# Kernel tuning notes

Measured on AMD Instinct MI355X. Metric: run time of the kernel, lower is better.

## Reference

```python
import jax, jax.numpy as jnp
import numpy as np

N, D, F, M, K = 4096, 1024, 4096, 2048, 307
EPS = 1e-5

def _ln(h, g, b):
    mu = jnp.mean(h, axis=-1, keepdims=True)
    var = jnp.mean(jnp.square(h - mu), axis=-1, keepdims=True)
    return (h - mu) * jax.lax.rsqrt(var + EPS) * g + b

def _attn(h, wq, wk, wv, mask):
    # wq/wk/wv stored as [D, D] so y = h @ w matches torch Linear(h) with W.T
    q = h @ wq
    k = h @ wk
    v = h @ wv
    s = (q @ k.T) * (1.0 / np.sqrt(D))  # [N, N]
    s = jnp.where(mask, -1e9, s)
    a = jax.nn.softmax(s, axis=-1)
    return a @ v, a

def _ffn(h, w1, b1, w2, b2):
    return jax.nn.gelu(h @ w1 + b1, approximate=False) @ w2 + b2

def setup_inputs() -> dict:
    ks = jax.random.split(jax.random.key(0), 32)
    s = 0.02
    p = lambda i, shape: (jax.random.normal(ks[i], shape, jnp.float32) * s)
    inp = {
        'x': jax.random.normal(ks[0], (N, D), jnp.float32),
        'real_edge_mask': jax.random.bernoulli(ks[1], 0.5, (N, N)),
        'fake_edge_mask': jax.random.bernoulli(ks[2], 0.5, (N, N)),
        'mask_nodes': jax.random.permutation(ks[3], N)[:M].astype(jnp.int32),
        'gene_idx': jnp.argsort(jax.random.uniform(ks[4], (M, D)), axis=-1)[:, :K].astype(jnp.int32),
        'wq1': p(5, (D, D)), 'wk1': p(6, (D, D)), 'wv1': p(7, (D, D)),
        'g1': jnp.ones((D,)), 'be1': jnp.zeros((D,)),
        'fw1': p(8, (D, F)), 'fb1': jnp.zeros((F,)),
        'fw2': p(9, (F, D)), 'fb2': jnp.zeros((D,)),
        'g2': jnp.ones((D,)), 'be2': jnp.zeros((D,)),
        'wq2': p(10, (D, D)), 'wk2': p(11, (D, D)), 'wv2': p(12, (D, D)),
        'g3': jnp.ones((D,)), 'be3': jnp.zeros((D,)),
        'hw1': p(13, (D, F)), 'hb1': jnp.zeros((F,)),
        'hw2': p(14, (F, D)), 'hb2': jnp.zeros((D,)),
        'g4': jnp.ones((D,)), 'be4': jnp.zeros((D,)),
        'head_w': p(15, (D, D)), 'head_b': jnp.zeros((D,)),
    }
    return inp

def reference(x, real_edge_mask, fake_edge_mask, mask_nodes, gene_idx,
              wq1, wk1, wv1, g1, be1, fw1, fb1, fw2, fb2, g2, be2,
              wq2, wk2, wv2, g3, be3, hw1, hb1, hw2, hb2, g4, be4,
              head_w, head_b):
    rows = jnp.arange(M)[:, None]  # [M, 1]
    # encoding_mask_nodes: zero K genes in each of M masked cells
    mask_x = x[mask_nodes].at[rows, gene_idx].set(0.0)
    use_x = x.at[mask_nodes].set(mask_x)

    hidden, encode_weights = _attn(use_x, wq1, wk1, wv1, real_edge_mask)
    hidden = _ln(hidden + use_x, g1, be1)
    hidden = _ln(hidden + _ffn(hidden, fw1, fb1, fw2, fb2), g2, be2)
    # NOTE: original `hidden[mask_nodes][gene_mask] = 0` is a no-op (copy), reproduced.

    recon, _decode_weights = _attn(hidden, wq2, wk2, wv2, real_edge_mask)
    recon = _ln(recon + hidden, g3, be3)
    recon = _ln(recon + _ffn(recon, hw1, hb1, hw2, hb2), g4, be4)
    h = recon @ head_w + head_b

    x_init = x[mask_nodes][rows, gene_idx]   # [M, K]
    x_recon = h[mask_nodes][rows, gene_idx]  # [M, K]
    return x_init, x_recon, encode_weights, recon
```

## Files before the change

### kernel.cpp

```cpp
#include <hip/hip_runtime.h>
#include <math.h>
#include <stdint.h>

typedef unsigned short u16;
typedef __attribute__((ext_vector_type(8))) short bf16x8;
typedef __attribute__((ext_vector_type(4))) float f32x4;

#define N_ 4096
#define D_ 1024
#define F_ 4096
#define M_ 2048
#define KG 307

__device__ __forceinline__ u16 f2bf(float f) {
  unsigned int u = __float_as_uint(f);
  unsigned int r = u + 0x7fffu + ((u >> 16) & 1u);
  return (u16)(r >> 16);
}

__device__ __forceinline__ float bf2f(u16 u) {
  return __uint_as_float((unsigned)u << 16);
}

__device__ __forceinline__ void gl_lds16(const u16* g, u16* l) {
  __builtin_amdgcn_global_load_lds(
      (__attribute__((address_space(1))) void*)(void*)g,
      (__attribute__((address_space(3))) void*)(void*)l,
      16, 0, 0);
}

enum { E_QKV = 0, E_SMASK = 1, E_PART = 2, E_GELU = 3 };
#define SMEM_BYTES 131072

template <int EPI>
__global__ __launch_bounds__(512, 2) void gemm256(
    const u16* __restrict__ A, const u16* __restrict__ B,
    void* __restrict__ C, void* __restrict__ C2,
    int gridM, int gridN, int Ndim, int Ksp, int lda, int ldb, long zstr,
    const float* __restrict__ bias, const unsigned char* __restrict__ mask,
    float scale) {
  extern __shared__ __align__(16) char smem[];
  const int tid = threadIdx.x;
  const int lane = tid & 63;
  const int wid = tid >> 6;
  const int wr = wid >> 2;
  const int wc = wid & 3;
  const int lr = lane & 15;
  const int lk = lane >> 4;

  const int nwg = gridM * gridN;
  const int bid = blockIdx.x;
  const int q8 = nwg >> 3, r8 = nwg & 7;
  const int xcd = bid & 7, ii = bid >> 3;
  int wg = (xcd < r8 ? xcd * (q8 + 1) : r8 * (q8 + 1) + (xcd - r8) * q8) + ii;
  const int rowblk = wg / (gridN << 2);
  const int rem = wg - rowblk * (gridN << 2);
  const int mrem = gridM - (rowblk << 2);
  int mtile, ntile;
  if (mrem >= 4) {
    ntile = rem >> 2;
    mtile = (rowblk << 2) + (rem & 3);
  } else {
    ntile = rem / mrem;
    mtile = (rowblk << 2) + (rem - ntile * mrem);
  }
  const long bm = (long)mtile * 256;
  const long bn = (long)ntile * 256;
  const long koff = (long)blockIdx.y * Ksp;
  const int NT = Ksp >> 6;

  auto stA = [&](int t, int h) {
    char* base = smem + ((t & 1) << 15) + (h << 14);
    const long k0 = koff + ((long)t << 6);
#pragma unroll
    for (int j = 0; j < 2; ++j) {
      int o = tid + (j << 9);
      int r = o >> 3, s = o & 7;
      gl_lds16(A + (bm + (h << 7) + r) * (long)lda + k0 + ((s ^ (r & 7)) << 3),
               (u16*)(base + o * 16));
    }
  };
  auto stB = [&](int t, int h) {
    char* base = smem + 65536 + ((t & 1) << 15) + (h << 14);
    const long k0 = koff + ((long)t << 6);
#pragma unroll
    for (int j = 0; j < 2; ++j) {
      int o = tid + (j << 9);
      int r = o >> 3, s = o & 7;
      gl_lds16(B + (bn + (h << 7) + r) * (long)ldb + k0 + ((s ^ (r & 7)) << 3),
               (u16*)(base + o * 16));
    }
  };

  bf16x8 avA[2][2], avB[2][2], bv[4][2];
  f32x4 acc[8][4];
#pragma unroll
  for (int m = 0; m < 8; ++m)
#pragma unroll
    for (int n = 0; n < 4; ++n) acc[m][n] = f32x4{0.f, 0.f, 0.f, 0.f};

  auto rdAV = [&](bf16x8(&av)[2][2], const char* Ab_, int q) {
#pragma unroll
    for (int e = 0; e < 2; ++e)
#pragma unroll
      for (int ks = 0; ks < 2; ++ks) {
        int r = (wr << 7) + (q << 5) + (e << 4) + lr;
        av[e][ks] = *(const bf16x8*)(Ab_ + r * 128 + ((((ks << 2) | lk) ^ (r & 7)) << 4));
      }
  };
  auto rdBV = [&](const char* Bb_) {
#pragma unroll
    for (int n = 0; n < 4; ++n)
#pragma unroll
      for (int ks = 0; ks < 2; ++ks) {
        int r = (wc << 6) + (n << 4) + lr;
        bv[n][ks] = *(const bf16x8*)(Bb_ + r * 128 + ((((ks << 2) | lk) ^ (r & 7)) << 4));
      }
  };

#define MM(Q, AV)                                                              \
  __builtin_amdgcn_s_setprio(1);                                               \
  _Pragma("unroll") for (int e = 0; e < 2; ++e)                                \
  _Pragma("unroll") for (int n = 0; n < 4; ++n)                                \
  _Pragma("unroll") for (int ks = 0; ks < 2; ++ks)                             \
      acc[((Q) << 1) | e][n] = __builtin_amdgcn_mfma_f32_16x16x32_bf16(        \
          AV[e][ks], bv[n][ks], acc[((Q) << 1) | e][n], 0, 0, 0);              \
  __builtin_amdgcn_s_setprio(0);                                               \
  __builtin_amdgcn_sched_barrier(0);

  stA(0, 0);
  stA(0, 1);
  stB(0, 0);
  stB(0, 1);
  if (NT > 1) {
    stB(1, 0);
    stB(1, 1);
  }
  __builtin_amdgcn_sched_barrier(0);
  if (NT > 1)
    asm volatile("s_waitcnt vmcnt(4)");
  else
    asm volatile("s_waitcnt vmcnt(0)");
  __builtin_amdgcn_sched_barrier(0);
  __builtin_amdgcn_s_barrier();
  rdAV(avA, smem, 0);
  __builtin_amdgcn_sched_barrier(0);

  for (int t = 0; t < NT; ++t) {
    const char* Ab = smem + ((t & 1) << 15);
    const char* AbN = smem + (((t + 1) & 1) << 15);
    const char* Bb = smem + 65536 + ((t & 1) << 15);
    rdBV(Bb);
    rdAV(avB, Ab, 1);
    if (t + 1 < NT) stA(t + 1, 0);
    __builtin_amdgcn_sched_barrier(0);
    asm volatile("s_waitcnt lgkmcnt(4)");
    __builtin_amdgcn_sched_barrier(0);
    MM(0, avA)
    rdAV(avA, Ab, 2);
    if (t + 1 < NT) stA(t + 1, 1);
    __builtin_amdgcn_sched_barrier(0);
    asm volatile("s_waitcnt lgkmcnt(4)");
    __builtin_amdgcn_sched_barrier(0);
    MM(1, avB)
    __builtin_amdgcn_s_barrier();
    rdAV(avB, Ab, 3);
    if (t + 2 < NT) stB(t + 2, 0);
    __builtin_amdgcn_sched_barrier(0);
    asm volatile("s_waitcnt lgkmcnt(4)");
    __builtin_amdgcn_sched_barrier(0);
    MM(2, avA)
    asm volatile("s_waitcnt lgkmcnt(0)");
    if (t + 2 < NT)
      asm volatile("s_waitcnt vmcnt(2)");
    else
      asm volatile("s_waitcnt vmcnt(0)");
    __builtin_amdgcn_sched_barrier(0);
    __builtin_amdgcn_s_barrier();
    if (t + 1 < NT) rdAV(avA, AbN, 0);
    if (t + 2 < NT) stB(t + 2, 1);
    __builtin_amdgcn_sched_barrier(0);
    MM(3, avB)
  }
#undef MM

  const bool z0 = (blockIdx.y == 0);
  float* Cz = (float*)C + (long)blockIdx.y * zstr;
#pragma unroll
  for (int m = 0; m < 8; ++m) {
#pragma unroll
    for (int n = 0; n < 4; ++n) {
#pragma unroll
      for (int j = 0; j < 4; ++j) {
        long row = bm + (wr << 7) + (m << 4) + (lk << 2) + j;
        long col = bn + (wc << 6) + (n << 4) + lr;
        float v = acc[m][n][j];
        if constexpr (EPI == E_QKV) {
          if (col < 2048)
            ((u16*)C)[row * 2048 + col] = f2bf(v);
          else
            ((u16*)C2)[(col - 2048) * (long)N_ + row] = f2bf(v);
        } else if constexpr (EPI == E_SMASK) {
          v *= scale;
          if (mask[row * Ndim + col]) v = -1e9f;
          ((u16*)C)[row * Ndim + col] = f2bf(v);
        } else if constexpr (EPI == E_PART) {
          Cz[row * Ndim + col] = v + ((z0 && bias) ? bias[col] : 0.f);
        } else if constexpr (EPI == E_GELU) {
          float tv = v + bias[col];
          float gl = 0.5f * tv * (1.0f + erff(tv * 0.70710678118654752f));
          ((u16*)C)[row * Ndim + col] = f2bf(gl);
        }
      }
    }
  }
}

__global__ __launch_bounds__(256) void gemm_nt_bias(
    const u16* __restrict__ A, const u16* __restrict__ B, float* __restrict__ C,
    int Ndim, int K, int lda, int ldb, const float* __restrict__ bias) {
  __shared__ u16 As[2][128 * 32];
  __shared__ u16 Bs[2][128 * 32];
  const int tid = threadIdx.x;
  const int lane = tid & 63;
  const int wid = tid >> 6;
  const int wr = wid >> 1;
  const int wc = wid & 1;
  const int lr = lane & 15;
  const int lk = lane >> 4;
  const long bm = (long)blockIdx.x * 128;
  const long bn = (long)blockIdx.y * 128;

  f32x4 acc[4][4];
#pragma unroll
  for (int i = 0; i < 4; ++i)
#pragma unroll
    for (int j = 0; j < 4; ++j) acc[i][j] = f32x4{0.f, 0.f, 0.f, 0.f};

  auto stage = [&](int buf, long k0) {
#pragma unroll
    for (int i = 0; i < 2; ++i) {
      int c = tid + i * 256;
      gl_lds16(A + (bm + (c >> 2)) * (long)lda + k0 + (c & 3) * 8, As[buf] + c * 8);
    }
#pragma unroll
    for (int i = 0; i < 2; ++i) {
      int c = tid + i * 256;
      gl_lds16(B + (bn + (c >> 2)) * (long)ldb + k0 + (c & 3) * 8, Bs[buf] + c * 8);
    }
  };

  stage(0, 0);
  __syncthreads();
  const int nt = K / 32;
  int cur = 0;
  for (int t = 0; t < nt; ++t) {
    if (t + 1 < nt) stage(cur ^ 1, (long)(t + 1) * 32);
    bf16x8 av[4], bv[4];
#pragma unroll
    for (int mr = 0; mr < 4; ++mr)
      av[mr] = *(const bf16x8*)(As[cur] + (wr * 64 + mr * 16 + lr) * 32 + lk * 8);
#pragma unroll
    for (int nr = 0; nr < 4; ++nr)
      bv[nr] = *(const bf16x8*)(Bs[cur] + (wc * 64 + nr * 16 + lr) * 32 + lk * 8);
#pragma unroll
    for (int mr = 0; mr < 4; ++mr)
#pragma unroll
      for (int nr = 0; nr < 4; ++nr)
        acc[mr][nr] = __builtin_amdgcn_mfma_f32_16x16x32_bf16(av[mr], bv[nr], acc[mr][nr], 0, 0, 0);
    __syncthreads();
    cur ^= 1;
  }
#pragma unroll
  for (int mr = 0; mr < 4; ++mr)
#pragma unroll
    for (int nr = 0; nr < 4; ++nr)
#pragma unroll
      for (int j = 0; j < 4; ++j) {
        long row = bm + wr * 64 + mr * 16 + lk * 4 + j;
        long col = bn + wc * 64 + nr * 16 + lr;
        C[row * Ndim + col] = acc[mr][nr][j] + bias[col];
      }
}

__global__ __launch_bounds__(256) void tcvt(const float* __restrict__ in,
                                            u16* __restrict__ out, int R, int C) {
  __shared__ float tile[32][33];
  int bx = blockIdx.x * 32;
  int by = blockIdx.y * 32;
  int tx = threadIdx.x & 31;
  int ty = threadIdx.x >> 5;
#pragma unroll
  for (int i = 0; i < 32; i += 8)
    tile[ty + i][tx] = in[(long)(by + ty + i) * C + bx + tx];
  __syncthreads();
#pragma unroll
  for (int i = 0; i < 32; i += 8)
    out[(long)(bx + ty + i) * R + by + tx] = f2bf(tile[tx][ty + i]);
}

__global__ void copy_usex(const float* __restrict__ x, float* __restrict__ xf,
                          u16* __restrict__ xb, long n) {
  long i = (long)blockIdx.x * blockDim.x + threadIdx.x;
  if (i < n) {
    float v = x[i];
    xf[i] = v;
    xb[i] = f2bf(v);
  }
}

__global__ void mask_zero(const float* __restrict__ x, const int* __restrict__ mask_nodes,
                          const int* __restrict__ gene_idx, float* __restrict__ xf,
                          u16* __restrict__ xb, float* __restrict__ x_init) {
  int m = blockIdx.x;
  int k = threadIdx.x;
  if (k >= KG) return;
  int row = mask_nodes[m];
  int col = gene_idx[m * KG + k];
  x_init[m * KG + k] = x[(long)row * D_ + col];
  xf[(long)row * D_ + col] = 0.f;
  xb[(long)row * D_ + col] = 0;
}

template <int NY>
__global__ __launch_bounds__(256) void add_ln(const float* __restrict__ y, long ystr,
                                              const float* __restrict__ r,
                                              const float* __restrict__ g,
                                              const float* __restrict__ b,
                                              float* __restrict__ of, u16* __restrict__ ob) {
  int row = blockIdx.x;
  const float* yr = y + (long)row * D_;
  const float* rr = r + (long)row * D_;
  float v[4];
  float s = 0.f, ss = 0.f;
#pragma unroll
  for (int i = 0; i < 4; ++i) {
    int idx = threadIdx.x + i * 256;
    float t = rr[idx];
#pragma unroll
    for (int z = 0; z < NY; ++z) t += yr[z * ystr + idx];
    v[i] = t;
    s += t;
    ss += t * t;
  }
#pragma unroll
  for (int o = 32; o > 0; o >>= 1) {
    s += __shfl_down(s, o, 64);
    ss += __shfl_down(ss, o, 64);
  }
  __shared__ float red[8];
  int wid = threadIdx.x >> 6, lane = threadIdx.x & 63;
  if (lane == 0) {
    red[wid] = s;
    red[4 + wid] = ss;
  }
  __syncthreads();
  if (threadIdx.x == 0) {
    red[0] = red[0] + red[1] + red[2] + red[3];
    red[4] = red[4] + red[5] + red[6] + red[7];
  }
  __syncthreads();
  float mu = red[0] * (1.f / D_);
  float var = red[4] * (1.f / D_) - mu * mu;
  float rs = rsqrtf(var + 1e-5f);
#pragma unroll
  for (int i = 0; i < 4; ++i) {
    int idx = threadIdx.x + i * 256;
    float o = (v[i] - mu) * rs * g[idx] + b[idx];
    of[(long)row * D_ + idx] = o;
    ob[(long)row * D_ + idx] = f2bf(o);
  }
}

template <bool WF32>
__global__ __launch_bounds__(256) void softmax_row(const u16* __restrict__ sin,
                                                   float* __restrict__ a32,
                                                   u16* __restrict__ a16) {
  int row = blockIdx.x;
  const long base = (long)row * N_ + threadIdx.x * 16;
  const u16* sr = sin + base;
  float v[16];
  bf16x8 h0 = *(const bf16x8*)(sr);
  bf16x8 h1 = *(const bf16x8*)(sr + 8);
#pragma unroll
  for (int j = 0; j < 8; ++j) {
    v[j] = bf2f((u16)h0[j]);
    v[8 + j] = bf2f((u16)h1[j]);
  }
  float mx = v[0];
#pragma unroll
  for (int i = 1; i < 16; ++i) mx = fmaxf(mx, v[i]);
#pragma unroll
  for (int o = 32; o > 0; o >>= 1) mx = fmaxf(mx, __shfl_down(mx, o, 64));
  __shared__ float red[8];
  int wid = threadIdx.x >> 6, lane = threadIdx.x & 63;
  if (lane == 0) red[wid] = mx;
  __syncthreads();
  if (threadIdx.x == 0) red[0] = fmaxf(fmaxf(red[0], red[1]), fmaxf(red[2], red[3]));
  __syncthreads();
  mx = red[0];
  float sum = 0.f;
#pragma unroll
  for (int i = 0; i < 16; ++i) {
    v[i] = __expf(v[i] - mx);
    sum += v[i];
  }
#pragma unroll
  for (int o = 32; o > 0; o >>= 1) sum += __shfl_down(sum, o, 64);
  if (lane == 0) red[4 + wid] = sum;
  __syncthreads();
  if (threadIdx.x == 0) red[4] = red[4] + red[5] + red[6] + red[7];
  __syncthreads();
  float inv = 1.f / red[4];
  bf16x8 o0, o1;
#pragma unroll
  for (int j = 0; j < 8; ++j) {
    float p0 = v[j] * inv, p1 = v[8 + j] * inv;
    o0[j] = (short)f2bf(p0);
    o1[j] = (short)f2bf(p1);
    if constexpr (WF32) {
      a32[base + j] = p0;
      a32[base + 8 + j] = p1;
    }
  }
  *(bf16x8*)(a16 + base) = o0;
  *(bf16x8*)(a16 + base + 8) = o1;
}

__global__ void gather_rows(const u16* __restrict__ src, const int* __restrict__ mask_nodes,
                            u16* __restrict__ dst) {
  int m = blockIdx.x;
  int row = mask_nodes[m];
  for (int i = threadIdx.x; i < D_; i += 256)
    dst[(long)m * D_ + i] = src[(long)row * D_ + i];
}

__global__ void gather_recon(const float* __restrict__ h, const int* __restrict__ gene_idx,
                             float* __restrict__ xr) {
  int m = blockIdx.x;
  int k = threadIdx.x;
  if (k >= KG) return;
  xr[m * KG + k] = h[(long)m * D_ + gene_idx[m * KG + k]];
}

extern "C" void kernel_launch(void* const* d_in, const int* in_sizes, int n_in,
                              void* d_out, int out_size, void* d_ws, size_t ws_size,
                              hipStream_t stream) {
  const float* x = (const float*)d_in[0];
  const unsigned char* real_mask = (const unsigned char*)d_in[1];
  const int* mask_nodes = (const int*)d_in[3];
  const int* gene_idx = (const int*)d_in[4];
  const float* wq1 = (const float*)d_in[5];
  const float* wk1 = (const float*)d_in[6];
  const float* wv1 = (const float*)d_in[7];
  const float* g1 = (const float*)d_in[8];
  const float* be1 = (const float*)d_in[9];
  const float* fw1 = (const float*)d_in[10];
  const float* fb1 = (const float*)d_in[11];
  const float* fw2 = (const float*)d_in[12];
  const float* fb2 = (const float*)d_in[13];
  const float* g2 = (const float*)d_in[14];
  const float* be2 = (const float*)d_in[15];
  const float* wq2 = (const float*)d_in[16];
  const float* wk2 = (const float*)d_in[17];
  const float* wv2 = (const float*)d_in[18];
  const float* g3 = (const float*)d_in[19];
  const float* be3 = (const float*)d_in[20];
  const float* hw1 = (const float*)d_in[21];
  const float* hb1 = (const float*)d_in[22];
  const float* hw2 = (const float*)d_in[23];
  const float* hb2 = (const float*)d_in[24];
  const float* g4 = (const float*)d_in[25];
  const float* be4 = (const float*)d_in[26];
  const float* head_w = (const float*)d_in[27];
  const float* head_b = (const float*)d_in[28];

  float* out_xinit = (float*)d_out;
  float* out_xrecon = out_xinit + (long)M_ * KG;
  float* out_enc = out_xrecon + (long)M_ * KG;
  float* out_recon = out_enc + (long)N_ * N_;

  hipFuncSetAttribute((const void*)gemm256<E_QKV>, hipFuncAttributeMaxDynamicSharedMemorySize, SMEM_BYTES);
  hipFuncSetAttribute((const void*)gemm256<E_SMASK>, hipFuncAttributeMaxDynamicSharedMemorySize, SMEM_BYTES);
  hipFuncSetAttribute((const void*)gemm256<E_PART>, hipFuncAttributeMaxDynamicSharedMemorySize, SMEM_BYTES);
  hipFuncSetAttribute((const void*)gemm256<E_GELU>, hipFuncAttributeMaxDynamicSharedMemorySize, SMEM_BYTES);

  char* w = (char*)d_ws;
  size_t off = 0;
  auto alloc = [&](size_t bytes) {
    void* p = w + off;
    off += (bytes + 255) & ~(size_t)255;
    return p;
  };
  float* useXf = (float*)alloc((size_t)N_ * D_ * 4);
  u16* useXb = (u16*)alloc((size_t)N_ * D_ * 2);
  u16* wslot = (u16*)alloc((size_t)D_ * F_ * 2);
  u16* qkb = (u16*)alloc((size_t)N_ * 2048 * 2);
  u16* vT = (u16*)alloc((size_t)D_ * N_ * 2);
  float* sbuf = (float*)alloc((size_t)N_ * N_ * 4);
  u16* aB = (u16*)alloc((size_t)N_ * N_ * 2);
  float* gout4 = (float*)alloc((size_t)4 * N_ * D_ * 4);
  float* actA = (float*)alloc((size_t)N_ * D_ * 4);
  float* actB = (float*)alloc((size_t)N_ * D_ * 4);
  u16* actB16 = (u16*)alloc((size_t)N_ * D_ * 2);
  u16* tbuf = (u16*)sbuf;
  u16* AgB = qkb;

  const float scale = 1.0f / 32.0f;
  const long nd = (long)N_ * D_;
  dim3 blk(256), blk5(512);

  copy_usex<<<dim3((unsigned)((nd + 255) / 256)), blk, 0, stream>>>(x, useXf, useXb, nd);
  mask_zero<<<dim3(M_), 320, 0, stream>>>(x, mask_nodes, gene_idx, useXf, useXb, out_xinit);

#define TCVT(src, R, C, dst) tcvt<<<dim3((C) / 32, (R) / 32), blk, 0, stream>>>(src, dst, R, C)
#define G256(EP, GM, GN, Z, A, B, C, C2, ND, KS, LA, LB, ZS, BI, MK, SC)                        \
  gemm256<EP><<<dim3((GM) * (GN), Z), blk5, SMEM_BYTES, stream>>>(A, B, C, C2, GM, GN, ND, KS, \
                                                                  LA, LB, ZS, BI, MK, SC)

  TCVT(wq1, D_, D_, wslot);
  TCVT(wk1, D_, D_, wslot + 1024 * 1024);
  TCVT(wv1, D_, D_, wslot + 2048 * 1024);
  G256(E_QKV, 16, 12, 1, useXb, wslot, qkb, vT, 3072, 1024, 1024, 1024, 0, nullptr, nullptr, 0.f);
  G256(E_SMASK, 16, 16, 1, qkb, qkb + 1024, aB, nullptr, 4096, 1024, 2048, 2048, 0, nullptr, real_mask, scale);
  softmax_row<true><<<dim3(N_), blk, 0, stream>>>(aB, out_enc, aB);
  G256(E_PART, 16, 4, 4, aB, vT, gout4, nullptr, 1024, 1024, 4096, 4096, nd, nullptr, nullptr, 0.f);
  add_ln<4><<<dim3(N_), blk, 0, stream>>>(gout4, nd, useXf, g1, be1, actA, actB16);
  TCVT(fw1, D_, F_, wslot);
  G256(E_GELU, 16, 16, 1, actB16, wslot, tbuf, nullptr, 4096, 1024, 1024, 1024, 0, fb1, nullptr, 0.f);
  TCVT(fw2, F_, D_, wslot);
  G256(E_PART, 16, 4, 4, tbuf, wslot, gout4, nullptr, 1024, 1024, 4096, 4096, nd, fb2, nullptr, 0.f);
  add_ln<4><<<dim3(N_), blk, 0, stream>>>(gout4, nd, actA, g2, be2, actB, actB16);

  TCVT(wq2, D_, D_, wslot);
  TCVT(wk2, D_, D_, wslot + 1024 * 1024);
  TCVT(wv2, D_, D_, wslot + 2048 * 1024);
  G256(E_QKV, 16, 12, 1, actB16, wslot, qkb, vT, 3072, 1024, 1024, 1024, 0, nullptr, nullptr, 0.f);
  G256(E_SMASK, 16, 16, 1, qkb, qkb + 1024, aB, nullptr, 4096, 1024, 2048, 2048, 0, nullptr, real_mask, scale);
  softmax_row<false><<<dim3(N_), blk, 0, stream>>>(aB, nullptr, aB);
  G256(E_PART, 16, 4, 4, aB, vT, gout4, nullptr, 1024, 1024, 4096, 4096, nd, nullptr, nullptr, 0.f);
  add_ln<4><<<dim3(N_), blk, 0, stream>>>(gout4, nd, actB, g3, be3, actA, actB16);
  TCVT(hw1, D_, F_, wslot);
  G256(E_GELU, 16, 16, 1, actB16, wslot, tbuf, nullptr, 4096, 1024, 1024, 1024, 0, hb1, nullptr, 0.f);
  TCVT(hw2, F_, D_, wslot);
  G256(E_PART, 16, 4, 4, tbuf, wslot, gout4, nullptr, 1024, 1024, 4096, 4096, nd, hb2, nullptr, 0.f);
  add_ln<4><<<dim3(N_), blk, 0, stream>>>(gout4, nd, actA, g4, be4, out_recon, actB16);

  gather_rows<<<dim3(M_), blk, 0, stream>>>(actB16, mask_nodes, AgB);
  TCVT(head_w, D_, D_, wslot);
  gemm_nt_bias<<<dim3(16, 8), blk, 0, stream>>>(AgB, wslot, gout4, 1024, 1024, 1024, 1024, head_b);
  gather_recon<<<dim3(M_), 320, 0, stream>>>(gout4, gene_idx, out_xrecon);
#undef TCVT
#undef G256
}
```

Before: 674.7 us.

## Use 128x128 tile GEMM with swizzled LDS for QKV and split-K GEMMs

Adds a gemm128 kernel with 128x128 tiles, an XOR-swizzled LDS layout and an XCD-aware block remap, and uses it for the QKV, attention-value, FFN-down and head GEMMs. The split-K factor for the 1024-wide-output GEMMs drops from 4 to 2, which halves the fp32 partial buffers that add_ln must reduce. The three QKV weight transposes are merged into one launch, and tbuf gets its own allocation. The aim is to fill more CUs on the narrow GEMMs and cut partial-sum traffic. The cost is that the simpler double-buffered kernel may reach lower per-CU MFMA efficiency than the tuned 256-tile kernel.

```diff
diff --git a/kernel.cpp b/kernel.cpp
--- a/kernel.cpp
+++ b/kernel.cpp
@@ -31,6 +31,105 @@
 
 enum { E_QKV = 0, E_SMASK = 1, E_PART = 2, E_GELU = 3 };
 #define SMEM_BYTES 131072
+
+template <int EPI>
+__global__ __launch_bounds__(256, 4) void gemm128(
+    const u16* __restrict__ A, const u16* __restrict__ B,
+    void* __restrict__ C, void* __restrict__ C2,
+    int Ndim, int Ksp, int lda, int ldb, long zstr,
+    const float* __restrict__ bias) {
+  __shared__ u16 As[2][128 * 32];
+  __shared__ u16 Bs[2][128 * 32];
+  const int tid = threadIdx.x;
+  const int lane = tid & 63;
+  const int wid = tid >> 6;
+  const int wr = wid >> 1;
+  const int wc = wid & 1;
+  const int lr = lane & 15;
+  const int lk = lane >> 4;
+
+  const int gx = gridDim.x, nwg = gx * gridDim.y;
+  const int bid = blockIdx.y * gx + blockIdx.x;
+  const int q8 = nwg >> 3, r8 = nwg & 7;
+  const int xcd = bid & 7, ii = bid >> 3;
+  const int wg = (xcd < r8 ? xcd * (q8 + 1) : r8 * (q8 + 1) + (xcd - r8) * q8) + ii;
+  const int mtile = wg % gx;
+  const int ntile = wg / gx;
+
+  const long bm = (long)mtile * 128;
+  const long bn = (long)ntile * 128;
+  const long koff = (long)blockIdx.z * Ksp;
+
+  f32x4 acc[4][4];
+#pragma unroll
+  for (int i = 0; i < 4; ++i)
+#pragma unroll
+    for (int j = 0; j < 4; ++j) acc[i][j] = f32x4{0.f, 0.f, 0.f, 0.f};
+
+  auto stage = [&](int buf, long k0) {
+#pragma unroll
+    for (int i = 0; i < 2; ++i) {
+      int o = tid + i * 256;
+      int r = o >> 2, s = o & 3;
+      gl_lds16(A + (bm + r) * (long)lda + k0 + ((s ^ ((r >> 1) & 3)) << 3), As[buf] + o * 8);
+    }
+#pragma unroll
+    for (int i = 0; i < 2; ++i) {
+      int o = tid + i * 256;
+      int r = o >> 2, s = o & 3;
+      gl_lds16(B + (bn + r) * (long)ldb + k0 + ((s ^ ((r >> 1) & 3)) << 3), Bs[buf] + o * 8);
+    }
+  };
+
+  stage(0, koff);
+  __syncthreads();
+  const int nt = Ksp / 32;
+  int cur = 0;
+  for (int t = 0; t < nt; ++t) {
+    if (t + 1 < nt) stage(cur ^ 1, koff + (long)(t + 1) * 32);
+    bf16x8 av[4], bv[4];
+#pragma unroll
+    for (int mr = 0; mr < 4; ++mr) {
+      int r = wr * 64 + mr * 16 + lr;
+      av[mr] = *(const bf16x8*)(As[cur] + r * 32 + ((lk ^ ((r >> 1) & 3)) << 3));
+    }
+#pragma unroll
+    for (int nr = 0; nr < 4; ++nr) {
+      int r = wc * 64 + nr * 16 + lr;
+      bv[nr] = *(const bf16x8*)(Bs[cur] + r * 32 + ((lk ^ ((r >> 1) & 3)) << 3));
+    }
+#pragma unroll
+    for (int mr = 0; mr < 4; ++mr)
+#pragma unroll
+      for (int nr = 0; nr < 4; ++nr)
+        acc[mr][nr] = __builtin_amdgcn_mfma_f32_16x16x32_bf16(av[mr], bv[nr], acc[mr][nr], 0, 0, 0);
+    __syncthreads();
+    cur ^= 1;
+  }
+
+  const bool z0 = (blockIdx.z == 0);
+  float* Cz = (float*)C + (long)blockIdx.z * zstr;
+#pragma unroll
+  for (int mr = 0; mr < 4; ++mr) {
+#pragma unroll
+    for (int nr = 0; nr < 4; ++nr) {
+#pragma unroll
+      for (int j = 0; j < 4; ++j) {
+        long row = bm + wr * 64 + mr * 16 + lk * 4 + j;
+        long col = bn + wc * 64 + nr * 16 + lr;
+        float v = acc[mr][nr][j];
+        if constexpr (EPI == E_QKV) {
+          if (col < 2048)
+            ((u16*)C)[row * 2048 + col] = f2bf(v);
+          else
+            ((u16*)C2)[(col - 2048) * (long)N_ + row] = f2bf(v);
+        } else if constexpr (EPI == E_PART) {
+          Cz[row * Ndim + col] = v + ((z0 && bias) ? bias[col] : 0.f);
+        }
+      }
+    }
+  }
+}
 
 template <int EPI>
 __global__ __launch_bounds__(512, 2) void gemm256(
@@ -184,8 +283,6 @@
   }
 #undef MM
 
-  const bool z0 = (blockIdx.y == 0);
-  float* Cz = (float*)C + (long)blockIdx.y * zstr;
 #pragma unroll
   for (int m = 0; m < 8; ++m) {
 #pragma unroll
@@ -195,17 +292,10 @@
         long row = bm + (wr << 7) + (m << 4) + (lk << 2) + j;
         long col = bn + (wc << 6) + (n << 4) + lr;
         float v = acc[m][n][j];
-        if constexpr (EPI == E_QKV) {
-          if (col < 2048)
-            ((u16*)C)[row * 2048 + col] = f2bf(v);
-          else
-            ((u16*)C2)[(col - 2048) * (long)N_ + row] = f2bf(v);
-        } else if constexpr (EPI == E_SMASK) {
+        if constexpr (EPI == E_SMASK) {
           v *= scale;
           if (mask[row * Ndim + col]) v = -1e9f;
           ((u16*)C)[row * Ndim + col] = f2bf(v);
-        } else if constexpr (EPI == E_PART) {
-          Cz[row * Ndim + col] = v + ((z0 && bias) ? bias[col] : 0.f);
         } else if constexpr (EPI == E_GELU) {
           float tv = v + bias[col];
           float gl = 0.5f * tv * (1.0f + erff(tv * 0.70710678118654752f));
@@ -216,76 +306,13 @@
   }
 }
 
-__global__ __launch_bounds__(256) void gemm_nt_bias(
-    const u16* __restrict__ A, const u16* __restrict__ B, float* __restrict__ C,
-    int Ndim, int K, int lda, int ldb, const float* __restrict__ bias) {
-  __shared__ u16 As[2][128 * 32];
-  __shared__ u16 Bs[2][128 * 32];
-  const int tid = threadIdx.x;
-  const int lane = tid & 63;
-  const int wid = tid >> 6;
-  const int wr = wid >> 1;
-  const int wc = wid & 1;
-  const int lr = lane & 15;
-  const int lk = lane >> 4;
-  const long bm = (long)blockIdx.x * 128;
-  const long bn = (long)blockIdx.y * 128;
-
-  f32x4 acc[4][4];
-#pragma unroll
-  for (int i = 0; i < 4; ++i)
-#pragma unroll
-    for (int j = 0; j < 4; ++j) acc[i][j] = f32x4{0.f, 0.f, 0.f, 0.f};
-
-  auto stage = [&](int buf, long k0) {
-#pragma unroll
-    for (int i = 0; i < 2; ++i) {
-      int c = tid + i * 256;
-      gl_lds16(A + (bm + (c >> 2)) * (long)lda + k0 + (c & 3) * 8, As[buf] + c * 8);
-    }
-#pragma unroll
-    for (int i = 0; i < 2; ++i) {
-      int c = tid + i * 256;
-      gl_lds16(B + (bn + (c >> 2)) * (long)ldb + k0 + (c & 3) * 8, Bs[buf] + c * 8);
-    }
-  };
-
-  stage(0, 0);
-  __syncthreads();
-  const int nt = K / 32;
-  int cur = 0;
-  for (int t = 0; t < nt; ++t) {
-    if (t + 1 < nt) stage(cur ^ 1, (long)(t + 1) * 32);
-    bf16x8 av[4], bv[4];
-#pragma unroll
-    for (int mr = 0; mr < 4; ++mr)
-      av[mr] = *(const bf16x8*)(As[cur] + (wr * 64 + mr * 16 + lr) * 32 + lk * 8);
-#pragma unroll
-    for (int nr = 0; nr < 4; ++nr)
-      bv[nr] = *(const bf16x8*)(Bs[cur] + (wc * 64 + nr * 16 + lr) * 32 + lk * 8);
-#pragma unroll
-    for (int mr = 0; mr < 4; ++mr)
-#pragma unroll
-      for (int nr = 0; nr < 4; ++nr)
-        acc[mr][nr] = __builtin_amdgcn_mfma_f32_16x16x32_bf16(av[mr], bv[nr], acc[mr][nr], 0, 0, 0);
-    __syncthreads();
-    cur ^= 1;
-  }
-#pragma unroll
-  for (int mr = 0; mr < 4; ++mr)
-#pragma unroll
-    for (int nr = 0; nr < 4; ++nr)
-#pragma unroll
-      for (int j = 0; j < 4; ++j) {
-        long row = bm + wr * 64 + mr * 16 + lk * 4 + j;
-        long col = bn + wc * 64 + nr * 16 + lr;
-        C[row * Ndim + col] = acc[mr][nr][j] + bias[col];
-      }
-}
-
-__global__ __launch_bounds__(256) void tcvt(const float* __restrict__ in,
-                                            u16* __restrict__ out, int R, int C) {
+__global__ __launch_bounds__(256) void tcvt3(const float* __restrict__ in0,
+                                             const float* __restrict__ in1,
+                                             const float* __restrict__ in2,
+                                             u16* __restrict__ out, int R, int C) {
   __shared__ float tile[32][33];
+  const float* in = (blockIdx.z == 0) ? in0 : (blockIdx.z == 1 ? in1 : in2);
+  u16* dst = out + (size_t)blockIdx.z * R * C;
   int bx = blockIdx.x * 32;
   int by = blockIdx.y * 32;
   int tx = threadIdx.x & 31;
@@ -296,7 +323,7 @@
   __syncthreads();
 #pragma unroll
   for (int i = 0; i < 32; i += 8)
-    out[(long)(bx + ty + i) * R + by + tx] = f2bf(tile[tx][ty + i]);
+    dst[(long)(bx + ty + i) * R + by + tx] = f2bf(tile[tx][ty + i]);
 }
 
 __global__ void copy_usex(const float* __restrict__ x, float* __restrict__ xf,
@@ -480,9 +507,7 @@
   float* out_enc = out_xrecon + (long)M_ * KG;
   float* out_recon = out_enc + (long)N_ * N_;
 
-  hipFuncSetAttribute((const void*)gemm256<E_QKV>, hipFuncAttributeMaxDynamicSharedMemorySize, SMEM_BYTES);
   hipFuncSetAttribute((const void*)gemm256<E_SMASK>, hipFuncAttributeMaxDynamicSharedMemorySize, SMEM_BYTES);
-  hipFuncSetAttribute((const void*)gemm256<E_PART>, hipFuncAttributeMaxDynamicSharedMemorySize, SMEM_BYTES);
   hipFuncSetAttribute((const void*)gemm256<E_GELU>, hipFuncAttributeMaxDynamicSharedMemorySize, SMEM_BYTES);
 
   char* w = (char*)d_ws;
@@ -497,13 +522,12 @@
   u16* wslot = (u16*)alloc((size_t)D_ * F_ * 2);
   u16* qkb = (u16*)alloc((size_t)N_ * 2048 * 2);
   u16* vT = (u16*)alloc((size_t)D_ * N_ * 2);
-  float* sbuf = (float*)alloc((size_t)N_ * N_ * 4);
+  u16* tbuf = (u16*)alloc((size_t)N_ * F_ * 2);
   u16* aB = (u16*)alloc((size_t)N_ * N_ * 2);
-  float* gout4 = (float*)alloc((size_t)4 * N_ * D_ * 4);
+  float* gout2 = (float*)alloc((size_t)2 * N_ * D_ * 4);
   float* actA = (float*)alloc((size_t)N_ * D_ * 4);
   float* actB = (float*)alloc((size_t)N_ * D_ * 4);
   u16* actB16 = (u16*)alloc((size_t)N_ * D_ * 2);
-  u16* tbuf = (u16*)sbuf;
   u16* AgB = qkb;
 
   const float scale = 1.0f / 32.0f;
@@ -513,43 +537,46 @@
   copy_usex<<<dim3((unsigned)((nd + 255) / 256)), blk, 0, stream>>>(x, useXf, useXb, nd);
   mask_zero<<<dim3(M_), 320, 0, stream>>>(x, mask_nodes, gene_idx, useXf, useXb, out_xinit);
 
-#define TCVT(src, R, C, dst) tcvt<<<dim3((C) / 32, (R) / 32), blk, 0, stream>>>(src, dst, R, C)
-#define G256(EP, GM, GN, Z, A, B, C, C2, ND, KS, LA, LB, ZS, BI, MK, SC)                        \
-  gemm256<EP><<<dim3((GM) * (GN), Z), blk5, SMEM_BYTES, stream>>>(A, B, C, C2, GM, GN, ND, KS, \
-                                                                  LA, LB, ZS, BI, MK, SC)
-
-  TCVT(wq1, D_, D_, wslot);
-  TCVT(wk1, D_, D_, wslot + 1024 * 1024);
-  TCVT(wv1, D_, D_, wslot + 2048 * 1024);
-  G256(E_QKV, 16, 12, 1, useXb, wslot, qkb, vT, 3072, 1024, 1024, 1024, 0, nullptr, nullptr, 0.f);
-  G256(E_SMASK, 16, 16, 1, qkb, qkb + 1024, aB, nullptr, 4096, 1024, 2048, 2048, 0, nullptr, real_mask, scale);
+#define TCVT1(src, R, C, dst) \
+  tcvt3<<<dim3((C) / 32, (R) / 32, 1), blk, 0, stream>>>(src, src, src, dst, R, C)
+#define TCVTQ(s0, s1, s2, dst) \
+  tcvt3<<<dim3(32, 32, 3), blk, 0, stream>>>(s0, s1, s2, dst, 1024, 1024)
+#define G128(EP, GM, GN, Z, A, B, C, C2, ND, KS, LA, LB, ZS, BI) \
+  gemm128<EP><<<dim3(GM, GN, Z), blk, 0, stream>>>(A, B, C, C2, ND, KS, LA, LB, ZS, BI)
+#define G256(EP, GM, GN, A, B, C, ND, KS, LA, LB, BI, MK, SC)                                \
+  gemm256<EP><<<dim3((GM) * (GN), 1), blk5, SMEM_BYTES, stream>>>(A, B, C, nullptr, GM, GN, \
+                                                                  ND, KS, LA, LB, 0, BI, MK, SC)
+
+  TCVTQ(wq1, wk1, wv1, wslot);
+  G128(E_QKV, 32, 24, 1, useXb, wslot, qkb, vT, 3072, 1024, 1024, 1024, 0, nullptr);
+  G256(E_SMASK, 16, 16, qkb, qkb + 1024, aB, 4096, 1024, 2048, 2048, nullptr, real_mask, scale);
   softmax_row<true><<<dim3(N_), blk, 0, stream>>>(aB, out_enc, aB);
-  G256(E_PART, 16, 4, 4, aB, vT, gout4, nullptr, 1024, 1024, 4096, 4096, nd, nullptr, nullptr, 0.f);
-  add_ln<4><<<dim3(N_), blk, 0, stream>>>(gout4, nd, useXf, g1, be1, actA, actB16);
-  TCVT(fw1, D_, F_, wslot);
-  G256(E_GELU, 16, 16, 1, actB16, wslot, tbuf, nullptr, 4096, 1024, 1024, 1024, 0, fb1, nullptr, 0.f);
-  TCVT(fw2, F_, D_, wslot);
-  G256(E_PART, 16, 4, 4, tbuf, wslot, gout4, nullptr, 1024, 1024, 4096, 4096, nd, fb2, nullptr, 0.f);
-  add_ln<4><<<dim3(N_), blk, 0, stream>>>(gout4, nd, actA, g2, be2, actB, actB16);
-
-  TCVT(wq2, D_, D_, wslot);
-  TCVT(wk2, D_, D_, wslot + 1024 * 1024);
-  TCVT(wv2, D_, D_, wslot + 2048 * 1024);
-  G256(E_QKV, 16, 12, 1, actB16, wslot, qkb, vT, 3072, 1024, 1024, 1024, 0, nullptr, nullptr, 0.f);
-  G256(E_SMASK, 16, 16, 1, qkb, qkb + 1024, aB, nullptr, 4096, 1024, 2048, 2048, 0, nullptr, real_mask, scale);
+  G128(E_PART, 32, 8, 2, aB, vT, gout2, nullptr, 1024, 2048, 4096, 4096, nd, nullptr);
+  add_ln<2><<<dim3(N_), blk, 0, stream>>>(gout2, nd, useXf, g1, be1, actA, actB16);
+  TCVT1(fw1, D_, F_, wslot);
+  G256(E_GELU, 16, 16, actB16, wslot, tbuf, 4096, 1024, 1024, 1024, fb1, nullptr, 0.f);
+  TCVT1(fw2, F_, D_, wslot);
+  G128(E_PART, 32, 8, 2, tbuf, wslot, gout2, nullptr, 1024, 2048, 4096, 4096, nd, fb2);
+  add_ln<2><<<dim3(N_), blk, 0, stream>>>(gout2, nd, actA, g2, be2, actB, actB16);
+
+  TCVTQ(wq2, wk2, wv2, wslot);
+  G128(E_QKV, 32, 24, 1, actB16, wslot, qkb, vT, 3072, 1024, 1024, 1024, 0, nullptr);
+  G256(E_SMASK, 16, 16, qkb, qkb + 1024, aB, 4096, 1024, 2048, 2048, nullptr, real_mask, scale);
   softmax_row<false><<<dim3(N_), blk, 0, stream>>>(aB, nullptr, aB);
-  G256(E_PART, 16, 4, 4, aB, vT, gout4, nullptr, 1024, 1024, 4096, 4096, nd, nullptr, nullptr, 0.f);
-  add_ln<4><<<dim3(N_), blk, 0, stream>>>(gout4, nd, actB, g3, be3, actA, actB16);
-  TCVT(hw1, D_, F_, wslot);
-  G256(E_GELU, 16, 16, 1, actB16, wslot, tbuf, nullptr, 4096, 1024, 1024, 1024, 0, hb1, nullptr, 0.f);
-  TCVT(hw2, F_, D_, wslot);
-  G256(E_PART, 16, 4, 4, tbuf, wslot, gout4, nullptr, 1024, 1024, 4096, 4096, nd, hb2, nullptr, 0.f);
-  add_ln<4><<<dim3(N_), blk, 0, stream>>>(gout4, nd, actA, g4, be4, out_recon, actB16);
+  G128(E_PART, 32, 8, 2, aB, vT, gout2, nullptr, 1024, 2048, 4096, 4096, nd, nullptr);
+  add_ln<2><<<dim3(N_), blk, 0, stream>>>(gout2, nd, actB, g3, be3, actA, actB16);
+  TCVT1(hw1, D_, F_, wslot);
+  G256(E_GELU, 16, 16, actB16, wslot, tbuf, 4096, 1024, 1024, 1024, hb1, nullptr, 0.f);
+  TCVT1(hw2, F_, D_, wslot);
+  G128(E_PART, 32, 8, 2, tbuf, wslot, gout2, nullptr, 1024, 2048, 4096, 4096, nd, hb2);
+  add_ln<2><<<dim3(N_), blk, 0, stream>>>(gout2, nd, actA, g4, be4, out_recon, actB16);
 
   gather_rows<<<dim3(M_), blk, 0, stream>>>(actB16, mask_nodes, AgB);
-  TCVT(head_w, D_, D_, wslot);
-  gemm_nt_bias<<<dim3(16, 8), blk, 0, stream>>>(AgB, wslot, gout4, 1024, 1024, 1024, 1024, head_b);
-  gather_recon<<<dim3(M_), 320, 0, stream>>>(gout4, gene_idx, out_xrecon);
-#undef TCVT
+  TCVT1(head_w, D_, D_, wslot);
+  G128(E_PART, 16, 8, 1, AgB, wslot, gout2, nullptr, 1024, 1024, 1024, 1024, 0, head_b);
+  gather_recon<<<dim3(M_), 320, 0, stream>>>(gout2, gene_idx, out_xrecon);
+#undef TCVT1
+#undef TCVTQ
+#undef G128
 #undef G256
 }
```

New measurement: 706.3 us. 4.7% more time.
